# Performance work log

Hardware: AMD Instinct MI355X
Metric: run time of the kernel (lower is better)

The kernel has to match this reference:

```python
import jax, jax.numpy as jnp
import numpy as np

HEADS = 4
BN_EPS = 1e-5


def setup_inputs() -> dict:
    key = jax.random.key(0)
    k1, k2, k3 = jax.random.split(key, 3)
    b, c, n = 4, 256, 4096
    x = jax.random.normal(k1, (b, c, n), dtype=jnp.float32)
    bn_weight = jnp.ones((c,), dtype=jnp.float32)
    bn_bias = jnp.zeros((c,), dtype=jnp.float32)
    # 1x1 Conv1d kernels are plain [out, in] matrices
    w_qkv = jax.random.normal(k2, (3 * c, c), dtype=jnp.float32) * (c ** -0.5)
    w_out = jax.random.normal(k3, (c, c), dtype=jnp.float32) * (c ** -0.5)
    b_out = jnp.zeros((c,), dtype=jnp.float32)
    return {"x": x, "bn_weight": bn_weight, "bn_bias": bn_bias,
            "w_qkv": w_qkv, "w_out": w_out, "b_out": b_out}


def reference(x, bn_weight, bn_bias, w_qkv, w_out, b_out):
    b, c, n = x.shape
    h = HEADS
    d = c // h
    scale = d ** -0.5

    # BatchNorm1d (training-mode batch statistics over batch and length dims)
    mean = jnp.mean(x, axis=(0, 2), keepdims=True)            # [1,c,1]
    var = jnp.var(x, axis=(0, 2), keepdims=True)
    xn = (x - mean) * jax.lax.rsqrt(var + BN_EPS)
    xn = xn * bn_weight[None, :, None] + bn_bias[None, :, None]

    # 1x1 conv QKV projection == matmul over channel dim
    qkv = jnp.einsum('oc,bcn->bon', w_qkv, xn)                # [b,3c,n]
    q, k, v = jnp.split(qkv, 3, axis=1)                       # each [b,c,n]
    # b (h d) n -> b h d n
    q = q.reshape(b, h, d, n) * scale
    k = k.reshape(b, h, d, n)
    v = v.reshape(b, h, d, n)

    attn = jax.nn.softmax(jnp.einsum('bhdi,bhdj->bhij', q, k), axis=-1)
    out = jnp.einsum('bhij,bhdj->bhid', attn, v)              # [b,h,n,d]
    # b h n d -> b (h d) n
    out = out.transpose(0, 1, 3, 2).reshape(b, c, n)
    return jnp.einsum('oc,bcn->bon', w_out, out) + b_out[None, :, None]
```

## Files before the change

### kernel.cpp

```cpp
#include <hip/hip_runtime.h>
#include <stdint.h>

#define B_ 4
#define C_ 256
#define N_ 4096
#define H_ 4
#define DH_ 64
#define BH_ 16
#define NTH 32

typedef __bf16 bf16x8 __attribute__((ext_vector_type(8)));
typedef float  f32x4  __attribute__((ext_vector_type(4)));
typedef float  f32x16 __attribute__((ext_vector_type(16)));
typedef unsigned short u16;

__device__ __forceinline__ u16 f2bf(float f) {
  uint32_t u = __float_as_uint(f);
  return (u16)((u + 0x7FFFu + ((u >> 16) & 1u)) >> 16);
}
__device__ __forceinline__ f32x4 mfma16(bf16x8 a, bf16x8 b, f32x4 c) {
  return __builtin_amdgcn_mfma_f32_16x16x32_bf16(a, b, c, 0, 0, 0);
}
__device__ __forceinline__ f32x16 mfma32(bf16x8 a, bf16x8 b, f32x16 c) {
  return __builtin_amdgcn_mfma_f32_32x32x16_bf16(a, b, c, 0, 0, 0);
}
__device__ __forceinline__ unsigned pk2(float a, float b) {
  unsigned r;
  asm("v_cvt_pk_bf16_f32 %0, %1, %2" : "=v"(r) : "v"(a), "v"(b));
  return r;
}
__device__ __forceinline__ float max3f(float a, float b, float c) {
  float r;
  asm("v_max3_f32 %0, %1, %2, %3" : "=v"(r) : "v"(a), "v"(b), "v"(c));
  return r;
}

__global__ __launch_bounds__(256) void k_prep(const float* __restrict__ x,
    u16* __restrict__ xT, float* __restrict__ s1p, float* __restrict__ s2p) {
  __shared__ float tile[64][65];
  int nbt = blockIdx.x, nb = nbt * 64, cb = blockIdx.y * 64, b = blockIdx.z;
  int t = threadIdx.x, col = t & 63, rq = t >> 6;
  int part = b * 64 + nbt;
  #pragma unroll
  for (int it = 0; it < 16; ++it) {
    int r = it * 4 + rq;
    float v = x[((size_t)b * C_ + cb + r) * N_ + nb + col];
    tile[r][col] = v;
    float s = v, sq = v * v;
    #pragma unroll
    for (int off = 32; off; off >>= 1) { s += __shfl_xor(s, off); sq += __shfl_xor(sq, off); }
    if (col == 0) {
      s1p[(size_t)(cb + r) * 256 + part] = s;
      s2p[(size_t)(cb + r) * 256 + part] = sq;
    }
  }
  __syncthreads();
  #pragma unroll
  for (int it = 0; it < 16; ++it) {
    int r = it * 4 + rq;
    xT[((size_t)b * N_ + nb + r) * C_ + cb + col] = f2bf(tile[col][r]);
  }
}

__global__ __launch_bounds__(256) void k_bnfin(const float* __restrict__ s1p,
    const float* __restrict__ s2p, const float* __restrict__ bw,
    const float* __restrict__ bbias, float* __restrict__ a, float* __restrict__ bb) {
  int ch = blockIdx.x, t = threadIdx.x;
  float s1 = s1p[(size_t)ch * 256 + t];
  float s2 = s2p[(size_t)ch * 256 + t];
  for (int off = 32; off; off >>= 1) { s1 += __shfl_xor(s1, off); s2 += __shfl_xor(s2, off); }
  __shared__ float r1[4], r2[4];
  if ((t & 63) == 0) { r1[t >> 6] = s1; r2[t >> 6] = s2; }
  __syncthreads();
  if (t == 0) {
    s1 = r1[0] + r1[1] + r1[2] + r1[3];
    s2 = r2[0] + r2[1] + r2[2] + r2[3];
    const float inv = 1.f / (B_ * N_);
    float mean = s1 * inv;
    float var  = s2 * inv - mean * mean;
    float av = bw[ch] * rsqrtf(var + 1e-5f);
    a[ch] = av;
    bb[ch] = bbias[ch] - mean * av;
  }
}

__global__ __launch_bounds__(256) void k_fold(const float* __restrict__ wq,
    const float* __restrict__ wo, const float* __restrict__ a, const float* __restrict__ bb,
    u16* __restrict__ wqf, float* __restrict__ qb, u16* __restrict__ woh) {
  int o = blockIdx.x, t = threadIdx.x;
  if (o < 3 * C_) {
    float w = wq[o * C_ + t];
    wqf[o * C_ + t] = f2bf(w * a[t]);
    float contrib = w * bb[t];
    for (int off = 32; off; off >>= 1) contrib += __shfl_down(contrib, off);
    __shared__ float r[4];
    if ((t & 63) == 0) r[t >> 6] = contrib;
    __syncthreads();
    if (t == 0) qb[o] = r[0] + r[1] + r[2] + r[3];
  } else {
    int oo = o - 3 * C_;
    woh[oo * C_ + t] = f2bf(wo[oo * C_ + t]);
  }
}

__global__ __launch_bounds__(256) void k_qkvgemm(const u16* __restrict__ xT,
    const u16* __restrict__ wqf, const float* __restrict__ qb,
    u16* __restrict__ q, u16* __restrict__ kk, u16* __restrict__ vtt) {
  __shared__ __align__(16) u16 As[128 * 64];
  __shared__ __align__(16) u16 Bs[128 * 64];
  int b = blockIdx.y;
  int bx = blockIdx.x;
  int mt = bx % 32, ot = bx / 32;
  int mbase = mt * 128, obase = ot * 128;
  int tid = threadIdx.x, w = tid >> 6, lane = tid & 63, lg = lane >> 4, lr = lane & 15;
  int wm = w >> 1, wn = w & 1;
  f32x4 acc[4][4] = {};
  const char* asrc = (const char*)xT + ((size_t)b * N_ + mbase) * 512;
  const char* bsrc = (const char*)wqf + (size_t)obase * 512;

  for (int ks = 0; ks < 4; ++ks) {
    int kbase = ks * 64;
    #pragma unroll
    for (int rr = 0; rr < 4; ++rr) {
      int p = tid * 16 + rr * 4096;
      int row = p >> 7, col = p & 127;
      int phys = p ^ ((row & 7) << 4);
      *(bf16x8*)((char*)As + phys) = *(const bf16x8*)(asrc + (size_t)row * 512 + kbase * 2 + col);
      *(bf16x8*)((char*)Bs + phys) = *(const bf16x8*)(bsrc + (size_t)row * 512 + kbase * 2 + col);
    }
    __syncthreads();
    #pragma unroll
    for (int kc = 0; kc < 2; ++kc) {
      bf16x8 af[4], bfr[4];
      #pragma unroll
      for (int i = 0; i < 4; ++i) {
        int r = wm * 64 + i * 16 + lr;
        int L = r * 128 + kc * 64 + lg * 16;
        af[i] = *(const bf16x8*)((const char*)As + (L ^ ((r & 7) << 4)));
        int rb = wn * 64 + i * 16 + lr;
        int Lb = rb * 128 + kc * 64 + lg * 16;
        bfr[i] = *(const bf16x8*)((const char*)Bs + (Lb ^ ((rb & 7) << 4)));
      }
      #pragma unroll
      for (int i = 0; i < 4; ++i)
        #pragma unroll
        for (int jj = 0; jj < 4; ++jj)
          acc[i][jj] = mfma16(af[i], bfr[jj], acc[i][jj]);
    }
    __syncthreads();
  }

  int s_id = (obase + wn * 64) >> 8;
  int h = ((obase + wn * 64) >> 6) & 3;
  int bh = b * H_ + h;
  float scale = (s_id == 0) ? 0.18033688011112042f : 1.f;
  #pragma unroll
  for (int i = 0; i < 4; ++i) {
    int n0 = mbase + wm * 64 + i * 16 + lg * 4;
    #pragma unroll
    for (int jj = 0; jj < 4; ++jj) {
      int o = obase + wn * 64 + jj * 16 + lr;
      int dd = jj * 16 + lr;
      float bias = qb[o];
      if (s_id == 2) {
        ushort4 pk;
        pk.x = f2bf(acc[i][jj][0] + bias);
        pk.y = f2bf(acc[i][jj][1] + bias);
        pk.z = f2bf(acc[i][jj][2] + bias);
        pk.w = f2bf(acc[i][jj][3] + bias);
        *(ushort4*)(vtt + ((size_t)bh * DH_ + dd) * N_ + n0) = pk;
      } else {
        u16* dst = (s_id == 0 ? q : kk) + (size_t)bh * N_ * DH_;
        #pragma unroll
        for (int r2 = 0; r2 < 4; ++r2)
          dst[(size_t)(n0 + r2) * DH_ + dd] = f2bf((acc[i][jj][r2] + bias) * scale);
      }
    }
  }
}

#define AS1 __attribute__((address_space(1)))
#define AS3 __attribute__((address_space(3)))

__global__ __launch_bounds__(256, 4) void k_attn(const u16* __restrict__ q,
    const u16* __restrict__ k, const u16* __restrict__ vt,
    u16* __restrict__ O0, u16* __restrict__ O1, float* __restrict__ lse) {
  __shared__ __align__(16) char kt_s[2][8192];
  __shared__ __align__(16) char vt_s[2][8192];
  int id = blockIdx.x;
  int xcd = id & 7, j = id >> 3;
  int bh = xcd * 2 + (j >> 6);
  int rem = j & 63;
  int qbase = (rem >> 1) * 128;
  int half = rem & 1;
  int tid = threadIdx.x, w = tid >> 6, lane = tid & 63;
  int l31 = lane & 31, hi = lane >> 5;

  const char* kg = (const char*)(k + ((size_t)bh * N_ + half * 2048) * DH_);
  const char* vg = (const char*)(vt + (size_t)bh * DH_ * N_ + half * 2048);

  int poff0 = w * 2048 + lane * 16;
  int poff1 = poff0 + 1024;
  int L0 = poff0 ^ (((poff0 >> 7) & 7) << 4);
  int L1 = poff1 ^ (((poff1 >> 7) & 7) << 4);
  const char* ks0 = kg + L0;
  const char* ks1 = kg + L1;
  const char* vs0 = vg + (size_t)(L0 >> 7) * 8192 + (L0 & 127);
  const char* vs1 = vg + (size_t)(L1 >> 7) * 8192 + (L1 & 127);

  bf16x8 bq[4];
  {
    const u16* qp = q + ((size_t)bh * N_ + qbase + w * 32 + l31) * DH_;
    #pragma unroll
    for (int cc = 0; cc < 4; ++cc)
      bq[cc] = *(const bf16x8*)(qp + cc * 16 + hi * 8);
  }

  f32x16 Oacc0, Oacc1;
  #pragma unroll
  for (int i = 0; i < 16; ++i) { Oacc0[i] = 0.f; Oacc1[i] = 0.f; }
  float m = -1e30f, l = 0.f;

  auto stage = [&](int par) {
    __builtin_amdgcn_global_load_lds((const AS1 void*)ks0,
        (AS3 void*)(kt_s[par] + w * 2048), 16, 0, 0);
    __builtin_amdgcn_global_load_lds((const AS1 void*)ks1,
        (AS3 void*)(kt_s[par] + w * 2048 + 1024), 16, 0, 0);
    __builtin_amdgcn_global_load_lds((const AS1 void*)vs0,
        (AS3 void*)(vt_s[par] + w * 2048), 16, 0, 0);
    __builtin_amdgcn_global_load_lds((const AS1 void*)vs1,
        (AS3 void*)(vt_s[par] + w * 2048 + 1024), 16, 0, 0);
    ks0 += 8192; ks1 += 8192; vs0 += 128; vs1 += 128;
  };

  auto body = [&](int kt, int par) {
    __syncthreads();
    if (kt + 1 < NTH) stage(par ^ 1);

    const char* kb = (const char*)kt_s[par];
    const char* vb = (const char*)vt_s[par];
    int vsw = (l31 & 7) << 4;

    #pragma unroll
    for (int st = 0; st < 2; ++st) {
      int rb = (st * 32 + l31) * 128;
      f32x16 s;
      #pragma unroll
      for (int i = 0; i < 16; ++i) s[i] = 0.f;
      __builtin_amdgcn_s_setprio(1);
      #pragma unroll
      for (int cc = 0; cc < 4; ++cc) {
        bf16x8 kf = *(const bf16x8*)(kb + ((rb + cc * 32 + hi * 16) ^ vsw));
        s = mfma32(kf, bq[cc], s);
      }
      __builtin_amdgcn_s_setprio(0);

      float a0 = max3f(s[0], s[1], s[2]);
      float a1 = max3f(s[3], s[4], s[5]);
      float a2 = max3f(s[6], s[7], s[8]);
      float a3 = max3f(s[9], s[10], s[11]);
      float a4 = max3f(s[12], s[13], s[14]);
      float b0 = max3f(a0, a1, s[15]);
      float b1 = max3f(a2, a3, a4);
      float mxloc = fmaxf(b0, b1);

      if (!__all(mxloc <= m + 8.f)) {
        float mx = fmaxf(mxloc, __shfl_xor(mxloc, 32));
        float mn = fmaxf(m, mx);
        float al = __builtin_amdgcn_exp2f(m - mn);
        m = mn; l *= al;
        #pragma unroll
        for (int i = 0; i < 16; ++i) { Oacc0[i] *= al; Oacc1[i] *= al; }
      }
      #pragma unroll
      for (int i = 0; i < 16; ++i) s[i] = __builtin_amdgcn_exp2f(s[i] - m);

      float u0 = s[0] + s[1], u1 = s[2] + s[3], u2 = s[4] + s[5], u3 = s[6] + s[7];
      float u4 = s[8] + s[9], u5 = s[10] + s[11], u6 = s[12] + s[13], u7 = s[14] + s[15];
      float v0 = u0 + u1, v1 = u2 + u3, v2 = u4 + u5, v3 = u6 + u7;
      float sum = (v0 + v1) + (v2 + v3);
      sum += __shfl_xor(sum, 32);
      l += sum;

      #pragma unroll
      for (int kslot = 0; kslot < 2; ++kslot) {
        const int a8 = kslot * 8;
        unsigned p0 = pk2(s[a8 + 0], s[a8 + 1]);
        unsigned p1 = pk2(s[a8 + 2], s[a8 + 3]);
        unsigned p2 = pk2(s[a8 + 4], s[a8 + 5]);
        unsigned p3 = pk2(s[a8 + 6], s[a8 + 7]);
        asm("v_permlane32_swap_b32 %0, %1" : "+v"(p0), "+v"(p2));
        asm("v_permlane32_swap_b32 %0, %1" : "+v"(p1), "+v"(p3));
        union { unsigned u[4]; bf16x8 b; } cv;
        cv.u[0] = p0; cv.u[1] = p1; cv.u[2] = p2; cv.u[3] = p3;
        bf16x8 pa = cv.b;
        int colb = (st * 2 + kslot) * 32 + hi * 16;
        __builtin_amdgcn_s_setprio(1);
        {
          bf16x8 vf = *(const bf16x8*)(vb + ((l31 * 128 + colb) ^ vsw));
          Oacc0 = mfma32(vf, pa, Oacc0);
        }
        {
          bf16x8 vf = *(const bf16x8*)(vb + (((32 + l31) * 128 + colb) ^ vsw));
          Oacc1 = mfma32(vf, pa, Oacc1);
        }
        __builtin_amdgcn_s_setprio(0);
      }
    }
  };

  stage(0);
  for (int kt = 0; kt < NTH; kt += 2) {
    body(kt, 0);
    body(kt + 1, 1);
  }

  float rl = 1.f / l;
  float lse_v = m + __builtin_amdgcn_logf(l);
  int qrow = qbase + w * 32 + l31;
  u16* dst = (half ? O1 : O0) + ((size_t)bh * N_ + qrow) * DH_;
  #pragma unroll
  for (int dt = 0; dt < 2; ++dt) {
    const f32x16& O = dt ? Oacc1 : Oacc0;
    #pragma unroll
    for (int rq = 0; rq < 4; ++rq) {
      ushort4 pk4;
      pk4.x = f2bf(O[rq * 4 + 0] * rl);
      pk4.y = f2bf(O[rq * 4 + 1] * rl);
      pk4.z = f2bf(O[rq * 4 + 2] * rl);
      pk4.w = f2bf(O[rq * 4 + 3] * rl);
      *(ushort4*)(dst + dt * 32 + rq * 8 + hi * 4) = pk4;
    }
  }
  if (hi == 0) lse[half * (BH_ * N_) + bh * N_ + qrow] = lse_v;
}

__global__ __launch_bounds__(256) void k_comb(const u16* __restrict__ O0,
    const u16* __restrict__ O1, const float* __restrict__ lse, u16* __restrict__ dst) {
  int t = blockIdx.x * 256 + threadIdx.x;
  int row = t >> 3, dp = (t & 7) * 8;
  float l0 = lse[row], l1 = lse[BH_ * N_ + row];
  float M = fmaxf(l0, l1);
  float w0 = __builtin_amdgcn_exp2f(l0 - M);
  float w1 = __builtin_amdgcn_exp2f(l1 - M);
  float inv = 1.f / (w0 + w1);
  w0 *= inv; w1 *= inv;
  uint4 a = *(const uint4*)(O0 + (size_t)row * 64 + dp);
  uint4 b = *(const uint4*)(O1 + (size_t)row * 64 + dp);
  uint4 o;
  #pragma unroll
  for (int i = 0; i < 4; ++i) {
    unsigned ua = (&a.x)[i], ub = (&b.x)[i];
    float alo = __uint_as_float(ua << 16), ahi = __uint_as_float(ua & 0xFFFF0000u);
    float blo = __uint_as_float(ub << 16), bhi = __uint_as_float(ub & 0xFFFF0000u);
    (&o.x)[i] = pk2(w0 * alo + w1 * blo, w0 * ahi + w1 * bhi);
  }
  *(uint4*)(dst + (size_t)row * 64 + dp) = o;
}

__global__ __launch_bounds__(256) void k_outgemm(const u16* __restrict__ ao,
    const u16* __restrict__ woh, const float* __restrict__ b_out,
    float* __restrict__ out) {
  __shared__ __align__(16) u16 As[128 * 64];
  __shared__ __align__(16) u16 Bs[128 * 64];
  int b = blockIdx.y;
  int bx = blockIdx.x;
  int mt = bx & 31, ot = bx >> 5;
  int mbase = mt * 128, obase = ot * 128;
  int tid = threadIdx.x, w = tid >> 6, lane = tid & 63, lg = lane >> 4, lr = lane & 15;
  int wm = w >> 1, wn = w & 1;
  f32x4 acc[4][4] = {};
  const char* bsrc = (const char*)woh + (size_t)obase * 512;

  for (int ks = 0; ks < 4; ++ks) {
    int kbase = ks * 64;
    int h = kbase >> 6;
    const char* asrc = (const char*)ao + ((size_t)(b * H_ + h) * N_ + mbase) * 128;
    #pragma unroll
    for (int rr = 0; rr < 4; ++rr) {
      int p = tid * 16 + rr * 4096;
      int row = p >> 7, col = p & 127;
      int phys = p ^ ((row & 7) << 4);
      *(bf16x8*)((char*)As + phys) = *(const bf16x8*)(asrc + p);
      *(bf16x8*)((char*)Bs + phys) = *(const bf16x8*)(bsrc + (size_t)row * 512 + kbase * 2 + col);
    }
    __syncthreads();
    #pragma unroll
    for (int kc = 0; kc < 2; ++kc) {
      bf16x8 af[4], bfr[4];
      #pragma unroll
      for (int i = 0; i < 4; ++i) {
        int r = wm * 64 + i * 16 + lr;
        int L = r * 128 + kc * 64 + lg * 16;
        af[i] = *(const bf16x8*)((const char*)As + (L ^ ((r & 7) << 4)));
        int rb = wn * 64 + i * 16 + lr;
        int Lb = rb * 128 + kc * 64 + lg * 16;
        bfr[i] = *(const bf16x8*)((const char*)Bs + (Lb ^ ((rb & 7) << 4)));
      }
      #pragma unroll
      for (int i = 0; i < 4; ++i)
        #pragma unroll
        for (int jj = 0; jj < 4; ++jj)
          acc[i][jj] = mfma16(af[i], bfr[jj], acc[i][jj]);
    }
    __syncthreads();
  }

  #pragma unroll
  for (int i = 0; i < 4; ++i) {
    int n0 = mbase + wm * 64 + i * 16 + lg * 4;
    #pragma unroll
    for (int jj = 0; jj < 4; ++jj) {
      int o = obase + wn * 64 + jj * 16 + lr;
      float bias = b_out[o];
      float4 vv = make_float4(acc[i][jj][0] + bias, acc[i][jj][1] + bias,
                              acc[i][jj][2] + bias, acc[i][jj][3] + bias);
      *(float4*)(out + ((size_t)(b * C_ + o)) * N_ + n0) = vv;
    }
  }
}

extern "C" void kernel_launch(void* const* d_in, const int* in_sizes, int n_in,
                              void* d_out, int out_size, void* d_ws, size_t ws_size,
                              hipStream_t stream) {
  const float* x    = (const float*)d_in[0];
  const float* bnw  = (const float*)d_in[1];
  const float* bnb  = (const float*)d_in[2];
  const float* wqkv = (const float*)d_in[3];
  const float* wout = (const float*)d_in[4];
  const float* bout = (const float*)d_in[5];
  float* out = (float*)d_out;
  char* ws = (char*)d_ws;

  float* a   = (float*)(ws + 0);
  float* bb  = (float*)(ws + 1024);
  float* qb  = (float*)(ws + 2048);
  u16* wqf = (u16*)(ws + 8192);
  u16* woh = (u16*)(ws + 8192 + 393216);
  const size_t big = 8388608;
  u16* xT  = (u16*)(ws + 532480);
  u16* q   = (u16*)(ws + 532480 + 1 * big);
  u16* kk  = (u16*)(ws + 532480 + 2 * big);
  u16* vt  = (u16*)(ws + 532480 + 3 * big);
  u16* ao  = (u16*)(ws + 532480 + 4 * big);
  const size_t tail = 532480 + 5 * big;
  float* s1p = (float*)(ws + tail);
  float* s2p = (float*)(ws + tail + 262144);
  float* lse = (float*)(ws + tail);

  k_prep   <<<dim3(64, 4, 4), 256, 0, stream>>>(x, xT, s1p, s2p);
  k_bnfin  <<<256, 256, 0, stream>>>(s1p, s2p, bnw, bnb, a, bb);
  k_fold   <<<1024, 256, 0, stream>>>(wqkv, wout, a, bb, wqf, qb, woh);
  k_qkvgemm<<<dim3(192, 4), 256, 0, stream>>>(xT, wqf, qb, q, kk, vt);
  k_attn   <<<dim3(1024), 256, 0, stream>>>(q, kk, vt, ao, xT, lse);
  k_comb   <<<dim3(2048), 256, 0, stream>>>(ao, xT, lse, ao);
  k_outgemm<<<dim3(64, 4), 256, 0, stream>>>(ao, woh, bout, out);
}
```

Before: 148.3 us.

## Fuse split-KV combine into output GEMM and restructure BN stats and softmax

Removes the separate combine kernel by merging the two split-KV partial outputs with their LSE weights while loading the A tile of the output GEMM. BatchNorm statistics move into a direct per-channel reduction kernel that reads x, replacing the partial-sum pass inside the transpose kernel. The attention inner loop folds the running max into the MFMA accumulator init and defers the cross-half row-sum shuffle to the end. The output GEMM now does extra exp and convert work per tile load, and the stats kernel reads x a second time with only 256 blocks.

```diff
diff --git a/kernel.cpp b/kernel.cpp
--- a/kernel.cpp
+++ b/kernel.cpp
@@ -35,42 +35,23 @@
   return r;
 }
 
-__global__ __launch_bounds__(256) void k_prep(const float* __restrict__ x,
-    u16* __restrict__ xT, float* __restrict__ s1p, float* __restrict__ s2p) {
-  __shared__ float tile[64][65];
-  int nbt = blockIdx.x, nb = nbt * 64, cb = blockIdx.y * 64, b = blockIdx.z;
-  int t = threadIdx.x, col = t & 63, rq = t >> 6;
-  int part = b * 64 + nbt;
-  #pragma unroll
-  for (int it = 0; it < 16; ++it) {
-    int r = it * 4 + rq;
-    float v = x[((size_t)b * C_ + cb + r) * N_ + nb + col];
-    tile[r][col] = v;
-    float s = v, sq = v * v;
-    #pragma unroll
-    for (int off = 32; off; off >>= 1) { s += __shfl_xor(s, off); sq += __shfl_xor(sq, off); }
-    if (col == 0) {
-      s1p[(size_t)(cb + r) * 256 + part] = s;
-      s2p[(size_t)(cb + r) * 256 + part] = sq;
-    }
-  }
-  __syncthreads();
-  #pragma unroll
-  for (int it = 0; it < 16; ++it) {
-    int r = it * 4 + rq;
-    xT[((size_t)b * N_ + nb + r) * C_ + cb + col] = f2bf(tile[col][r]);
-  }
-}
-
-__global__ __launch_bounds__(256) void k_bnfin(const float* __restrict__ s1p,
-    const float* __restrict__ s2p, const float* __restrict__ bw,
-    const float* __restrict__ bbias, float* __restrict__ a, float* __restrict__ bb) {
+__global__ __launch_bounds__(256) void k_bnstats(const float* __restrict__ x,
+    const float* __restrict__ bw, const float* __restrict__ bbias,
+    float* __restrict__ a, float* __restrict__ bb) {
   int ch = blockIdx.x, t = threadIdx.x;
-  float s1 = s1p[(size_t)ch * 256 + t];
-  float s2 = s2p[(size_t)ch * 256 + t];
-  for (int off = 32; off; off >>= 1) { s1 += __shfl_xor(s1, off); s2 += __shfl_xor(s2, off); }
+  float s1 = 0.f, s2 = 0.f;
+  for (int b = 0; b < B_; ++b) {
+    const float4* p = (const float4*)(x + ((size_t)b * C_ + ch) * N_);
+    for (int i = t; i < N_ / 4; i += 256) {
+      float4 v = p[i];
+      s1 += v.x + v.y + v.z + v.w;
+      s2 += v.x * v.x + v.y * v.y + v.z * v.z + v.w * v.w;
+    }
+  }
+  for (int off = 32; off; off >>= 1) { s1 += __shfl_down(s1, off); s2 += __shfl_down(s2, off); }
   __shared__ float r1[4], r2[4];
-  if ((t & 63) == 0) { r1[t >> 6] = s1; r2[t >> 6] = s2; }
+  int w = t >> 6;
+  if ((t & 63) == 0) { r1[w] = s1; r2[w] = s2; }
   __syncthreads();
   if (t == 0) {
     s1 = r1[0] + r1[1] + r1[2] + r1[3];
@@ -100,6 +81,25 @@
   } else {
     int oo = o - 3 * C_;
     woh[oo * C_ + t] = f2bf(wo[oo * C_ + t]);
+  }
+}
+
+__global__ __launch_bounds__(256) void k_transpose(const float* __restrict__ x,
+                                                   u16* __restrict__ xT) {
+  __shared__ float tile[64][65];
+  int nb = blockIdx.x * 64, cb = blockIdx.y * 64, b = blockIdx.z;
+  int t = threadIdx.x;
+  int col = t & 63, rq = t >> 6;
+  #pragma unroll
+  for (int it = 0; it < 16; ++it) {
+    int r = it * 4 + rq;
+    tile[r][col] = x[((size_t)b * C_ + cb + r) * N_ + nb + col];
+  }
+  __syncthreads();
+  #pragma unroll
+  for (int it = 0; it < 16; ++it) {
+    int r = it * 4 + rq;
+    xT[((size_t)b * N_ + nb + r) * C_ + cb + col] = f2bf(tile[col][r]);
   }
 }
 
@@ -219,7 +219,7 @@
   f32x16 Oacc0, Oacc1;
   #pragma unroll
   for (int i = 0; i < 16; ++i) { Oacc0[i] = 0.f; Oacc1[i] = 0.f; }
-  float m = -1e30f, l = 0.f;
+  float m = 0.f, l = 0.f;
 
   auto stage = [&](int par) {
     __builtin_amdgcn_global_load_lds((const AS1 void*)ks0,
@@ -245,8 +245,9 @@
     for (int st = 0; st < 2; ++st) {
       int rb = (st * 32 + l31) * 128;
       f32x16 s;
-      #pragma unroll
-      for (int i = 0; i < 16; ++i) s[i] = 0.f;
+      float negm = -m;
+      #pragma unroll
+      for (int i = 0; i < 16; ++i) s[i] = negm;
       __builtin_amdgcn_s_setprio(1);
       #pragma unroll
       for (int cc = 0; cc < 4; ++cc) {
@@ -264,23 +265,23 @@
       float b1 = max3f(a2, a3, a4);
       float mxloc = fmaxf(b0, b1);
 
-      if (!__all(mxloc <= m + 8.f)) {
+      if (!__all(mxloc <= 8.f)) {
         float mx = fmaxf(mxloc, __shfl_xor(mxloc, 32));
-        float mn = fmaxf(m, mx);
-        float al = __builtin_amdgcn_exp2f(m - mn);
-        m = mn; l *= al;
+        float delta = fmaxf(mx, 0.f);
+        float al = __builtin_amdgcn_exp2f(-delta);
+        m += delta; l *= al;
+        #pragma unroll
+        for (int i = 0; i < 16; ++i) s[i] -= delta;
         #pragma unroll
         for (int i = 0; i < 16; ++i) { Oacc0[i] *= al; Oacc1[i] *= al; }
       }
       #pragma unroll
-      for (int i = 0; i < 16; ++i) s[i] = __builtin_amdgcn_exp2f(s[i] - m);
+      for (int i = 0; i < 16; ++i) s[i] = __builtin_amdgcn_exp2f(s[i]);
 
       float u0 = s[0] + s[1], u1 = s[2] + s[3], u2 = s[4] + s[5], u3 = s[6] + s[7];
       float u4 = s[8] + s[9], u5 = s[10] + s[11], u6 = s[12] + s[13], u7 = s[14] + s[15];
       float v0 = u0 + u1, v1 = u2 + u3, v2 = u4 + u5, v3 = u6 + u7;
-      float sum = (v0 + v1) + (v2 + v3);
-      sum += __shfl_xor(sum, 32);
-      l += sum;
+      l += (v0 + v1) + (v2 + v3);
 
       #pragma unroll
       for (int kslot = 0; kslot < 2; ++kslot) {
@@ -315,6 +316,7 @@
     body(kt + 1, 1);
   }
 
+  l += __shfl_xor(l, 32);
   float rl = 1.f / l;
   float lse_v = m + __builtin_amdgcn_logf(l);
   int qrow = qbase + w * 32 + l31;
@@ -335,30 +337,8 @@
   if (hi == 0) lse[half * (BH_ * N_) + bh * N_ + qrow] = lse_v;
 }
 
-__global__ __launch_bounds__(256) void k_comb(const u16* __restrict__ O0,
-    const u16* __restrict__ O1, const float* __restrict__ lse, u16* __restrict__ dst) {
-  int t = blockIdx.x * 256 + threadIdx.x;
-  int row = t >> 3, dp = (t & 7) * 8;
-  float l0 = lse[row], l1 = lse[BH_ * N_ + row];
-  float M = fmaxf(l0, l1);
-  float w0 = __builtin_amdgcn_exp2f(l0 - M);
-  float w1 = __builtin_amdgcn_exp2f(l1 - M);
-  float inv = 1.f / (w0 + w1);
-  w0 *= inv; w1 *= inv;
-  uint4 a = *(const uint4*)(O0 + (size_t)row * 64 + dp);
-  uint4 b = *(const uint4*)(O1 + (size_t)row * 64 + dp);
-  uint4 o;
-  #pragma unroll
-  for (int i = 0; i < 4; ++i) {
-    unsigned ua = (&a.x)[i], ub = (&b.x)[i];
-    float alo = __uint_as_float(ua << 16), ahi = __uint_as_float(ua & 0xFFFF0000u);
-    float blo = __uint_as_float(ub << 16), bhi = __uint_as_float(ub & 0xFFFF0000u);
-    (&o.x)[i] = pk2(w0 * alo + w1 * blo, w0 * ahi + w1 * bhi);
-  }
-  *(uint4*)(dst + (size_t)row * 64 + dp) = o;
-}
-
-__global__ __launch_bounds__(256) void k_outgemm(const u16* __restrict__ ao,
+__global__ __launch_bounds__(256) void k_outgemm(const u16* __restrict__ O0,
+    const u16* __restrict__ O1, const float* __restrict__ lse,
     const u16* __restrict__ woh, const float* __restrict__ b_out,
     float* __restrict__ out) {
   __shared__ __align__(16) u16 As[128 * 64];
@@ -375,13 +355,33 @@
   for (int ks = 0; ks < 4; ++ks) {
     int kbase = ks * 64;
     int h = kbase >> 6;
-    const char* asrc = (const char*)ao + ((size_t)(b * H_ + h) * N_ + mbase) * 128;
+    int bh = b * H_ + h;
+    const char* a0 = (const char*)O0 + ((size_t)bh * N_ + mbase) * 128;
+    const char* a1 = (const char*)O1 + ((size_t)bh * N_ + mbase) * 128;
+    const float* lp0 = lse + (size_t)bh * N_ + mbase;
+    const float* lp1 = lp0 + (size_t)BH_ * N_;
     #pragma unroll
     for (int rr = 0; rr < 4; ++rr) {
       int p = tid * 16 + rr * 4096;
       int row = p >> 7, col = p & 127;
       int phys = p ^ ((row & 7) << 4);
-      *(bf16x8*)((char*)As + phys) = *(const bf16x8*)(asrc + p);
+      float e0 = lp0[row], e1 = lp1[row];
+      float Mx = fmaxf(e0, e1);
+      float w0 = __builtin_amdgcn_exp2f(e0 - Mx);
+      float w1 = __builtin_amdgcn_exp2f(e1 - Mx);
+      float inv = 1.f / (w0 + w1);
+      w0 *= inv; w1 *= inv;
+      uint4 av = *(const uint4*)(a0 + p);
+      uint4 bv = *(const uint4*)(a1 + p);
+      uint4 o;
+      #pragma unroll
+      for (int i = 0; i < 4; ++i) {
+        unsigned ua = (&av.x)[i], ub = (&bv.x)[i];
+        float alo = __uint_as_float(ua << 16), ahi = __uint_as_float(ua & 0xFFFF0000u);
+        float blo = __uint_as_float(ub << 16), bhi = __uint_as_float(ub & 0xFFFF0000u);
+        (&o.x)[i] = pk2(w0 * alo + w1 * blo, w0 * ahi + w1 * bhi);
+      }
+      *(uint4*)((char*)As + phys) = o;
       *(bf16x8*)((char*)Bs + phys) = *(const bf16x8*)(bsrc + (size_t)row * 512 + kbase * 2 + col);
     }
     __syncthreads();
@@ -442,17 +442,13 @@
   u16* q   = (u16*)(ws + 532480 + 1 * big);
   u16* kk  = (u16*)(ws + 532480 + 2 * big);
   u16* vt  = (u16*)(ws + 532480 + 3 * big);
-  u16* ao  = (u16*)(ws + 532480 + 4 * big);
-  const size_t tail = 532480 + 5 * big;
-  float* s1p = (float*)(ws + tail);
-  float* s2p = (float*)(ws + tail + 262144);
-  float* lse = (float*)(ws + tail);
-
-  k_prep   <<<dim3(64, 4, 4), 256, 0, stream>>>(x, xT, s1p, s2p);
-  k_bnfin  <<<256, 256, 0, stream>>>(s1p, s2p, bnw, bnb, a, bb);
-  k_fold   <<<1024, 256, 0, stream>>>(wqkv, wout, a, bb, wqf, qb, woh);
-  k_qkvgemm<<<dim3(192, 4), 256, 0, stream>>>(xT, wqf, qb, q, kk, vt);
-  k_attn   <<<dim3(1024), 256, 0, stream>>>(q, kk, vt, ao, xT, lse);
-  k_comb   <<<dim3(2048), 256, 0, stream>>>(ao, xT, lse, ao);
-  k_outgemm<<<dim3(64, 4), 256, 0, stream>>>(ao, woh, bout, out);
-}
+  u16* O0  = (u16*)(ws + 532480 + 4 * big);
+  float* lse = (float*)(ws + 532480 + 5 * big);
+
+  k_bnstats <<<256, 256, 0, stream>>>(x, bnw, bnb, a, bb);
+  k_fold    <<<1024, 256, 0, stream>>>(wqkv, wout, a, bb, wqf, qb, woh);
+  k_transpose<<<dim3(64, 4, 4), 256, 0, stream>>>(x, xT);
+  k_qkvgemm <<<dim3(192, 4), 256, 0, stream>>>(xT, wqf, qb, q, kk, vt);
+  k_attn    <<<dim3(1024), 256, 0, stream>>>(q, kk, vt, O0, xT, lse);
+  k_outgemm <<<dim3(64, 4), 256, 0, stream>>>(O0, xT, lse, woh, bout, out);
+}
```

Result: no change. 146.0 us (-1.5%).
